# Optimization experiments

Hardware: AMD Instinct MI355X
Metric: run time of the kernel (lower is better)

Reference implementation:

```python
import jax, jax.numpy as jnp
import numpy as np

N_HEADS = 16
EPS = 1e-6  # WanSelfAttention passes eps=1e-6 to WanRMSNorm
ROPE_MAX = 1024


def _rmsnorm(v, g):
    # WanRMSNorm: normalize in fp32 over the full `dim`, then scale by weight
    v32 = v.astype(jnp.float32)
    n = v32 * jax.lax.rsqrt(jnp.mean(v32 * v32, axis=-1, keepdims=True) + EPS)
    return n * g


def _rope(x, f, h, w, fc, fs):
    # x: [b, s, n, d] with s == f*h*w. Complex rope: (a+bi) * (cos + i sin)
    b, s, n, d = x.shape
    c = d // 2
    c1 = c - 2 * (c // 3)
    c2 = c // 3

    def build(t):  # t: [ROPE_MAX, c] -> [1, s, 1, c]
        tf, th, tw = t[:, :c1], t[:, c1:c1 + c2], t[:, c1 + c2:]
        pf = jnp.broadcast_to(tf[:f, None, None, :], (f, h, w, c1))
        ph = jnp.broadcast_to(th[None, :h, None, :], (f, h, w, c2))
        pw = jnp.broadcast_to(tw[None, None, :w, :], (f, h, w, c2))
        return jnp.concatenate([pf, ph, pw], axis=-1).reshape(1, f * h * w, 1, c)

    cosv, sinv = build(fc), build(fs)
    xr = x.astype(jnp.float32).reshape(b, s, n, c, 2)
    a, bi = xr[..., 0], xr[..., 1]
    out_r = a * cosv - bi * sinv
    out_i = a * sinv + bi * cosv
    return jnp.stack([out_r, out_i], axis=-1).reshape(b, s, n, d)


def setup_inputs() -> dict:
    key = jax.random.key(0)
    ks = jax.random.split(key, 12)
    b, s, dim = 1, 2048, 2048
    n, d = N_HEADS, 2048 // N_HEADS  # d = 128, c = 64
    f, h, w = 2, 32, 32              # f*h*w == s
    c = d // 2
    c1 = c - 2 * (c // 3)
    c2 = c // 3

    # Realistic rope tables per band (cos/sin of pos * inv_freq)
    pos = np.arange(ROPE_MAX, dtype=np.float64)[:, None]
    ang = []
    for cx in (c1, c2, c2):
        inv = 1.0 / (10000.0 ** (np.arange(cx, dtype=np.float64) / cx))
        ang.append(pos * inv[None, :])
    ang = np.concatenate(ang, axis=1)
    freqs_cos = jnp.asarray(np.cos(ang), dtype=jnp.float32)
    freqs_sin = jnp.asarray(np.sin(ang), dtype=jnp.float32)

    scale = 1.0 / np.sqrt(dim)
    inp = {
        "x": jax.random.normal(ks[0], (b, s, dim), dtype=jnp.float32),
        "freqs_cos": freqs_cos,
        "freqs_sin": freqs_sin,
        "Wq": jax.random.normal(ks[1], (dim, dim), dtype=jnp.float32) * scale,
        "bq": jnp.zeros((dim,), dtype=jnp.float32),
        "Wk": jax.random.normal(ks[2], (dim, dim), dtype=jnp.float32) * scale,
        "bk": jnp.zeros((dim,), dtype=jnp.float32),
        "Wv": jax.random.normal(ks[3], (dim, dim), dtype=jnp.float32) * scale,
        "bv": jnp.zeros((dim,), dtype=jnp.float32),
        "Wo": jax.random.normal(ks[4], (dim, dim), dtype=jnp.float32) * scale,
        "bo": jnp.zeros((dim,), dtype=jnp.float32),
        "gq": jnp.ones((dim,), dtype=jnp.float32),
        "gk": jnp.ones((dim,), dtype=jnp.float32),
        "seq_lens": jnp.array([s], dtype=jnp.int32),
        "f": f,
        "h": h,
        "w": w,
    }
    return inp


def reference(x, freqs_cos, freqs_sin, Wq, bq, Wk, bk, Wv, bv, Wo, bo, gq, gk,
              seq_lens, f, h, w):
    b, s, dim = x.shape
    n = N_HEADS
    d = dim // n

    q = _rmsnorm(x @ Wq.T + bq, gq).reshape(b, s, n, d)
    k = _rmsnorm(x @ Wk.T + bk, gk).reshape(b, s, n, d)
    v = (x @ Wv.T + bv).reshape(b, s, n, d)

    q = _rope(q, f, h, w, freqs_cos, freqs_sin)
    k = _rope(k, f, h, w, freqs_cos, freqs_sin)

    scale = np.float32(1.0 / np.sqrt(d))
    scores = jnp.einsum('bqnd,bknd->bnqk', q, k) * scale  # [b,n,s,s]
    key_mask = jnp.arange(s)[None, :] < seq_lens[:, None]  # [b,s] (k_lens)
    scores = jnp.where(key_mask[:, None, None, :], scores, -jnp.inf)
    probs = jax.nn.softmax(scores, axis=-1)
    out = jnp.einsum('bnqk,bknd->bqnd', probs, v).reshape(b, s, dim)
    return out @ Wo.T + bo
```

## Files before the change

kernel.cpp:

```cpp
#include <hip/hip_runtime.h>
#include <cstdint>
#include <cmath>

typedef unsigned int uint;
typedef unsigned short ushort;
typedef __bf16 bf16_t;
typedef bf16_t bf16x8 __attribute__((ext_vector_type(8)));
typedef float f32x4 __attribute__((ext_vector_type(4)));
typedef float f32x16 __attribute__((ext_vector_type(16)));

#define LOG2E 1.44269504088896340736f

__device__ __forceinline__ ushort f2bf(float f) {
  uint x = __float_as_uint(f);
  x += 0x7fffu + ((x >> 16) & 1u);
  return (ushort)(x >> 16);
}
__device__ __forceinline__ uint pack2(float lo, float hi) {
  return (uint)f2bf(lo) | ((uint)f2bf(hi) << 16);
}
__device__ __forceinline__ uint cvt_pk_bf16(float lo, float hi) {
  uint r;
  asm("v_cvt_pk_bf16_f32 %0, %1, %2" : "=v"(r) : "v"(lo), "v"(hi));
  return r;
}

__device__ __forceinline__ void gload_lds16(const void* gsrc, void* ldsdst) {
  typedef const __attribute__((address_space(1))) unsigned int* gp_t;
  typedef __attribute__((address_space(3))) unsigned int* lp_t;
  __builtin_amdgcn_global_load_lds((gp_t)(uintptr_t)gsrc,
                                   (lp_t)(unsigned int)(uintptr_t)ldsdst,
                                   16, 0, 0);
}

__global__ __launch_bounds__(256) void cvt5(const float* __restrict__ x,
                                            const float* __restrict__ wq,
                                            const float* __restrict__ wk,
                                            const float* __restrict__ wv,
                                            const float* __restrict__ wo,
                                            ushort* __restrict__ xb,
                                            ushort* __restrict__ wqkv,
                                            ushort* __restrict__ wob,
                                            int nx8, int nw8) {
  const int y = blockIdx.y;
  const float* src;
  ushort* dst;
  int n8;
  if (y == 0)      { src = x;  dst = xb;  n8 = nx8; }
  else if (y == 4) { src = wo; dst = wob; n8 = nw8; }
  else {
    src = (y == 1) ? wq : (y == 2) ? wk : wv;
    dst = wqkv + (size_t)(y - 1) * nw8 * 8;
    n8 = nw8;
  }
  int i = blockIdx.x * blockDim.x + threadIdx.x;
  if (i >= n8) return;
  const float4* s4 = (const float4*)src;
  float4 a = s4[i * 2], b = s4[i * 2 + 1];
  uint4 o;
  o.x = pack2(a.x, a.y); o.y = pack2(a.z, a.w);
  o.z = pack2(b.x, b.y); o.w = pack2(b.z, b.w);
  ((uint4*)dst)[i] = o;
}

__global__ __launch_bounds__(512) void gemm_qkv192(const ushort* __restrict__ A,
                                                   const ushort* __restrict__ B,
                                                   const float* __restrict__ bq,
                                                   const float* __restrict__ bk,
                                                   const float* __restrict__ bv,
                                                   float* __restrict__ qpre,
                                                   float* __restrict__ kpre,
                                                   ushort* __restrict__ Vt,
                                                   int K, int S_) {
  __shared__ __align__(16) unsigned char ldsA[65536];
  __shared__ __align__(16) unsigned char ldsB[49152];
  const int t = threadIdx.x, l = t & 63;
  const int w = t >> 6;
  const int g = l >> 4, c = l & 15;
  const int wr = w >> 2, wc = w & 3;
  const int tm = blockIdx.y * 256, tn = blockIdx.x * 192;

  const int srow = t >> 3;
  const int schunk = (t & 7) ^ (srow & 7);
  const ushort* Ag = A + (size_t)(tm + srow) * K + schunk * 8;
  const ushort* Bg = B + (size_t)(tn + srow) * K + schunk * 8;
  const size_t rK64 = (size_t)64 * K;

#define STG_A(kt, u) gload_lds16(Ag + (size_t)(u) * rK64 + ((kt) << 6),   \
    ldsA + ((kt)&1) * 32768 + (u) * 8192 + t * 16)
#define STG_B(kt, u) gload_lds16(Bg + (size_t)(u) * rK64 + ((kt) << 6),   \
    ldsB + ((kt)&1) * 24576 + (u) * 8192 + t * 16)

  f32x4 acc[8][3] = {};
  bf16x8 af[2][2], bfr[3][2];
  const int cr = c * 128;
  const int sw0 = ((0 * 4 + g) ^ (c & 7)) << 4;
  const int sw1 = ((1 * 4 + g) ^ (c & 7)) << 4;

#define RDA(d, q) do {                                                               \
    _Pragma("unroll") for (int mm = 0; mm < 2; ++mm) {                               \
      const unsigned char* p_ = ldsA + (d)*32768 + (wr*128 + (q)*32 + mm*16)*128 + cr; \
      af[mm][0] = *(const bf16x8*)(p_ + sw0);                                        \
      af[mm][1] = *(const bf16x8*)(p_ + sw1); }                                      \
  } while (0)
#define RDB(d) do {                                                                 \
    _Pragma("unroll") for (int nn = 0; nn < 3; ++nn) {                              \
      const unsigned char* p_ = ldsB + (d)*24576 + (wc*48 + nn*16)*128 + cr;        \
      bfr[nn][0] = *(const bf16x8*)(p_ + sw0);                                      \
      bfr[nn][1] = *(const bf16x8*)(p_ + sw1); }                                    \
  } while (0)
#define MM(q) do {                                                                  \
    __builtin_amdgcn_s_setprio(1);                                                  \
    _Pragma("unroll") for (int mm = 0; mm < 2; ++mm)                                \
    _Pragma("unroll") for (int nn = 0; nn < 3; ++nn) {                              \
      acc[(q)*2+mm][nn] = __builtin_amdgcn_mfma_f32_16x16x32_bf16(                  \
          af[mm][0], bfr[nn][0], acc[(q)*2+mm][nn], 0, 0, 0);                       \
      acc[(q)*2+mm][nn] = __builtin_amdgcn_mfma_f32_16x16x32_bf16(                  \
          af[mm][1], bfr[nn][1], acc[(q)*2+mm][nn], 0, 0, 0); }                     \
    __builtin_amdgcn_s_setprio(0);                                                  \
  } while (0)
#define BAR() __builtin_amdgcn_s_barrier()

  STG_B(0, 0); STG_B(0, 1); STG_B(0, 2);
  STG_A(0, 0); STG_A(0, 1); STG_A(0, 2); STG_A(0, 3);
  STG_B(1, 0); STG_B(1, 1); STG_B(1, 2);
  STG_A(1, 0); STG_A(1, 1); STG_A(1, 2);
  asm volatile("s_waitcnt vmcnt(6)" ::: "memory");
  BAR();

  const int NITER = K >> 7;
  for (int i = 0; i < NITER; ++i) {
    const int k1 = 2 * i + 1, k2 = 2 * i + 2, k3 = 2 * i + 3;
    const bool st = (i + 1 < NITER);
    RDA(0, 0); RDB(0);
    STG_A(k1, 3);
    MM(0); BAR();
    RDA(0, 1);
    if (st) { STG_B(k2, 0); STG_B(k2, 1); }
    MM(1); BAR();
    RDA(0, 2);
    if (st) { STG_B(k2, 2); STG_A(k2, 0); }
    MM(2); BAR();
    RDA(0, 3);
    if (st) { STG_A(k2, 1); STG_A(k2, 2); }
    MM(3);
    if (st) asm volatile("s_waitcnt vmcnt(6)" ::: "memory");
    else    asm volatile("s_waitcnt vmcnt(0)" ::: "memory");
    BAR();
    RDA(1, 0); RDB(1);
    if (st) STG_A(k2, 3);
    MM(0); BAR();
    RDA(1, 1);
    if (st) { STG_B(k3, 0); STG_B(k3, 1); }
    MM(1); BAR();
    RDA(1, 2);
    if (st) { STG_B(k3, 2); STG_A(k3, 0); }
    MM(2); BAR();
    RDA(1, 3);
    if (st) { STG_A(k3, 1); STG_A(k3, 2); }
    MM(3);
    if (st) asm volatile("s_waitcnt vmcnt(6)" ::: "memory");
    else    asm volatile("s_waitcnt vmcnt(0)" ::: "memory");
    BAR();
  }

#undef STG_A
#undef STG_B
#undef RDA
#undef RDB
#undef MM
#undef BAR

#pragma unroll
  for (int n = 0; n < 3; ++n) {
    int col = tn + wc * 48 + n * 16 + c;
    int sel = col >> 11;
    if (sel < 2) {
      float* outp = sel ? kpre : qpre;
      const float* bias = sel ? bk : bq;
      int col2 = col & 2047;
      float bvv = bias[col2];
#pragma unroll
      for (int m = 0; m < 8; ++m) {
        int row0 = tm + wr * 128 + m * 16 + g * 4;
#pragma unroll
        for (int i = 0; i < 4; ++i)
          outp[(size_t)(row0 + i) * 2048 + col2] = acc[m][n][i] + bvv;
      }
    } else {
      int colv = col - 4096;
      float bvv = bv[colv];
#pragma unroll
      for (int m = 0; m < 8; ++m) {
        int row0 = tm + wr * 128 + m * 16 + g * 4;
        uint2 o;
        o.x = pack2(acc[m][n][0] + bvv, acc[m][n][1] + bvv);
        o.y = pack2(acc[m][n][2] + bvv, acc[m][n][3] + bvv);
        *(uint2*)(Vt + (size_t)colv * S_ + row0) = o;
      }
    }
  }
}

__global__ __launch_bounds__(512) void gemm_wo_db(const ushort* __restrict__ A,
                                                  const ushort* __restrict__ B,
                                                  float* __restrict__ pbuf, int K) {
  __shared__ __align__(16) unsigned char As[16384];
  __shared__ __align__(16) unsigned char Bs[16384];
  const int t = threadIdx.x, l = t & 63, w = t >> 6;
  const int g = l >> 4, c = l & 15;
  const int wr = w >> 1, wc = w & 1;
  const int tm = blockIdx.y * 128, tn = blockIdx.x * 128;
  const int ks = blockIdx.z;
  const int k0 = ks * (K >> 1);

  const int srow = w * 16 + (l >> 2);
  const int schunk = (l & 3) ^ (srow & 3);
  const ushort* Ag = A + (size_t)(tm + srow) * K + k0 + schunk * 8;
  const ushort* Bg = B + (size_t)(tn + srow) * K + k0 + schunk * 8;

  f32x4 acc[2][4] = {};

  const int NT = K >> 6;
  gload_lds16(Ag, As + w * 1024);
  gload_lds16(Bg, Bs + w * 1024);

  for (int j = 0; j < NT; ++j) {
    const int buf = j & 1, nb = buf ^ 1;
    if (j + 1 < NT) {
      const int kt1 = (j + 1) << 5;
      gload_lds16(Ag + kt1, As + nb * 8192 + w * 1024);
      gload_lds16(Bg + kt1, Bs + nb * 8192 + w * 1024);
      asm volatile("s_waitcnt vmcnt(2)" ::: "memory");
    } else {
      asm volatile("s_waitcnt vmcnt(0)" ::: "memory");
    }
    __builtin_amdgcn_s_barrier();

    const unsigned char* Ab = As + buf * 8192;
    const unsigned char* Bb = Bs + buf * 8192;
    bf16x8 af[2], bfr[4];
#pragma unroll
    for (int m = 0; m < 2; ++m) {
      int row = wr * 32 + m * 16 + c;
      af[m] = *(const bf16x8*)(Ab + row * 64 + ((g ^ (row & 3)) << 4));
    }
#pragma unroll
    for (int n = 0; n < 4; ++n) {
      int row = wc * 64 + n * 16 + c;
      bfr[n] = *(const bf16x8*)(Bb + row * 64 + ((g ^ (row & 3)) << 4));
    }
#pragma unroll
    for (int m = 0; m < 2; ++m)
#pragma unroll
      for (int n = 0; n < 4; ++n)
        acc[m][n] = __builtin_amdgcn_mfma_f32_16x16x32_bf16(af[m], bfr[n], acc[m][n], 0, 0, 0);

    __builtin_amdgcn_s_barrier();
  }

  float* out = pbuf + (size_t)ks * 2048 * 2048;
#pragma unroll
  for (int n = 0; n < 4; ++n) {
    int col = tn + wc * 64 + n * 16 + c;
#pragma unroll
    for (int m = 0; m < 2; ++m) {
      int row0 = tm + wr * 32 + m * 16 + g * 4;
#pragma unroll
      for (int i = 0; i < 4; ++i)
        out[(size_t)(row0 + i) * 2048 + col] = acc[m][n][i];
    }
  }
}

__global__ __launch_bounds__(256) void reduce_wo(const float* __restrict__ p,
                                                 const float* __restrict__ bo,
                                                 float* __restrict__ out, int n4) {
  int i = blockIdx.x * blockDim.x + threadIdx.x;
  if (i >= n4) return;
  float4 a = ((const float4*)p)[i];
  float4 b = ((const float4*)p)[i + n4];
  float4 bb = *(const float4*)(bo + ((i * 4) & 2047));
  float4 o;
  o.x = a.x + b.x + bb.x; o.y = a.y + b.y + bb.y;
  o.z = a.z + b.z + bb.z; o.w = a.w + b.w + bb.w;
  ((float4*)out)[i] = o;
}

__global__ __launch_bounds__(256) void fuse_rms_rope(const float* __restrict__ qpre,
                                                     const float* __restrict__ kpre,
                                                     const float* __restrict__ gq,
                                                     const float* __restrict__ gk,
                                                     const float* __restrict__ fc,
                                                     const float* __restrict__ fs,
                                                     const int* __restrict__ pH,
                                                     const int* __restrict__ pW,
                                                     ushort* __restrict__ Qb,
                                                     ushort* __restrict__ Kb,
                                                     int dim, float foldq) {
  const int which = blockIdx.y;
  const float* pre = which ? kpre : qpre;
  const float* gw = which ? gk : gq;
  ushort* outp = which ? Kb : Qb;
  const float fold = which ? 1.0f : foldq;

  const int p = blockIdx.x, t = threadIdx.x;
  const float* row = pre + (size_t)p * dim;
  float v[8];
  {
    float4 a = *(const float4*)(row + t * 8);
    float4 b = *(const float4*)(row + t * 8 + 4);
    v[0] = a.x; v[1] = a.y; v[2] = a.z; v[3] = a.w;
    v[4] = b.x; v[5] = b.y; v[6] = b.z; v[7] = b.w;
  }
  float ss = 0.f;
#pragma unroll
  for (int i = 0; i < 8; ++i) ss += v[i] * v[i];
#pragma unroll
  for (int off = 32; off; off >>= 1) ss += __shfl_xor(ss, off);
  __shared__ float wsum[4];
  if ((t & 63) == 0) wsum[t >> 6] = ss;
  __syncthreads();
  float rstd = rsqrtf((wsum[0] + wsum[1] + wsum[2] + wsum[3]) * (1.0f / dim) + 1e-6f);
  float gv[8];
  {
    float4 a = *(const float4*)(gw + t * 8);
    float4 b = *(const float4*)(gw + t * 8 + 4);
    gv[0] = a.x; gv[1] = a.y; gv[2] = a.z; gv[3] = a.w;
    gv[4] = b.x; gv[5] = b.y; gv[6] = b.z; gv[7] = b.w;
  }
#pragma unroll
  for (int i = 0; i < 8; ++i) v[i] = v[i] * rstd * gv[i];

  const int H = pH[0], W = pW[0];
  const int hw = H * W;
  const int fr = p / hw;
  const int rem = p - fr * hw;
  const int hh = rem / W;
  const int ww = rem - hh * W;
  const int hd = dim / 16;
  const int cd = hd >> 1;
  const int c2 = cd / 3, c1 = cd - 2 * c2;
  const int j0 = ((t * 8) % hd) >> 1;

  uint ob[4];
#pragma unroll
  for (int q = 0; q < 4; ++q) {
    int j = j0 + q;
    int ri = (j < c1) ? fr : ((j < c1 + c2) ? hh : ww);
    float cs = fc[ri * cd + j];
    float sn = fs[ri * cd + j];
    float a = v[2 * q], b = v[2 * q + 1];
    ob[q] = pack2((a * cs - b * sn) * fold, (a * sn + b * cs) * fold);
  }
  uint4 o4; o4.x = ob[0]; o4.y = ob[1]; o4.z = ob[2]; o4.w = ob[3];
  *(uint4*)(outp + (size_t)p * dim + t * 8) = o4;
}

__global__ __launch_bounds__(512, 2) void attn32(const ushort* __restrict__ Qb,
                                                 const ushort* __restrict__ Kb,
                                                 const ushort* __restrict__ Vt,
                                                 ushort* __restrict__ Ob,
                                                 const int* __restrict__ seq_lens,
                                                 int S_, int DIMc) {
  __shared__ __align__(16) unsigned char smem[66560];
  float* mlbuf = (float*)(smem + 65536);
  const int t = threadIdx.x, l = t & 63, w = t >> 6;
  const int qsub = w & 3, ksp = w >> 2;
  const int h = l >> 5, ql = l & 31;

  const int orig = blockIdx.y * gridDim.x + blockIdx.x;
  const int nwg = gridDim.x * gridDim.y;
  const int lin = (orig & 7) * (nwg >> 3) + (orig >> 3);
  const int q0 = (lin % gridDim.x) * 128;
  const int head = lin / gridDim.x;
  const int kvlen = seq_lens[0];

  unsigned char* sk_s = smem + ksp * 16384;
  unsigned char* sv_s = smem + 32768 + ksp * 16384;

  bf16x8 qf[8];
  {
    const ushort* qp = Qb + (size_t)(q0 + qsub * 32 + ql) * DIMc + head * 128 + h * 8;
#pragma unroll
    for (int s = 0; s < 8; ++s) qf[s] = *(const bf16x8*)(qp + s * 16);
  }

  f32x16 ofr[4] = {};
  float m_run = -1e30f, l_run = 0.f;

  const int nt = (kvlen + 63) >> 6;
  const int half = (nt + 1) >> 1;
  const int tbase = ksp ? half : 0;
  const int mycnt = ksp ? (nt - half) : half;

  for (int tt = 0; tt < half; ++tt) {
    __syncthreads();
    if (tt < mycnt) {
      const int kv0 = (tbase + tt) * 64;
#pragma unroll
      for (int it = 0; it < 4; ++it) {
        int kr = qsub * 16 + it * 4 + (l >> 4);
        int kc = (l & 15) ^ (kr & 15);
        gload_lds16(Kb + (size_t)(kv0 + kr) * DIMc + head * 128 + kc * 8,
                    sk_s + qsub * 4096 + it * 1024);
        int vr = qsub * 32 + it * 8 + (l >> 3);
        int vc = (l & 7) ^ (vr & 7);
        gload_lds16(Vt + (size_t)(head * 128 + vr) * S_ + kv0 + vc * 8,
                    sv_s + qsub * 4096 + it * 1024);
      }
    }
    __syncthreads();
    if (tt >= mycnt) continue;
    const int kv0 = (tbase + tt) * 64;

    f32x16 sfr[2] = {};
    __builtin_amdgcn_s_setprio(1);
#pragma unroll
    for (int kb = 0; kb < 2; ++kb) {
      const unsigned char* kbp = sk_s + (kb * 32 + ql) * 256;
      const int rx = (kb * 32 + ql) & 15;
#pragma unroll
      for (int s = 0; s < 8; ++s) {
        bf16x8 kf = *(const bf16x8*)(kbp + (((s * 2 + h) ^ rx) << 4));
        sfr[kb] = __builtin_amdgcn_mfma_f32_32x32x16_bf16(kf, qf[s], sfr[kb], 0, 0, 0);
      }
    }
    __builtin_amdgcn_s_setprio(0);

    if (kv0 + 64 > kvlen) {
#pragma unroll
      for (int kb = 0; kb < 2; ++kb)
#pragma unroll
        for (int r = 0; r < 16; ++r) {
          int key = kv0 + kb * 32 + (r & 3) + 8 * (r >> 2) + 4 * h;
          if (key >= kvlen) sfr[kb][r] = -1e30f;
        }
    }

    float mt = -1e30f;
#pragma unroll
    for (int kb = 0; kb < 2; ++kb)
#pragma unroll
      for (int r = 0; r < 16; ++r) mt = fmaxf(mt, sfr[kb][r]);
    mt = fmaxf(mt, __shfl_xor(mt, 32));

    if (!__all(mt <= m_run + 8.0f)) {
      float m_new = fmaxf(m_run, mt);
      float fac = __builtin_amdgcn_exp2f(m_run - m_new);
      l_run *= fac;
#pragma unroll
      for (int df = 0; df < 4; ++df) ofr[df] *= fac;
      m_run = m_new;
    }

    float ls = 0.f;
    uint u[2][4][2];
#pragma unroll
    for (int kb = 0; kb < 2; ++kb)
#pragma unroll
      for (int G = 0; G < 4; ++G) {
        float p0 = __builtin_amdgcn_exp2f(sfr[kb][G * 4 + 0] - m_run);
        float p1 = __builtin_amdgcn_exp2f(sfr[kb][G * 4 + 1] - m_run);
        float p2 = __builtin_amdgcn_exp2f(sfr[kb][G * 4 + 2] - m_run);
        float p3 = __builtin_amdgcn_exp2f(sfr[kb][G * 4 + 3] - m_run);
        ls += (p0 + p1) + (p2 + p3);
        u[kb][G][0] = cvt_pk_bf16(p0, p1);
        u[kb][G][1] = cvt_pk_bf16(p2, p3);
      }
    ls += __shfl_xor(ls, 32);
    l_run += ls;

#pragma unroll
    for (int ks = 0; ks < 4; ++ks) {
      const int kb = ks >> 1, G0 = (ks & 1) * 2;
      uint own0 = h ? u[kb][G0 + 1][0] : u[kb][G0][0];
      uint own1 = h ? u[kb][G0 + 1][1] : u[kb][G0][1];
      uint snd0 = h ? u[kb][G0][0] : u[kb][G0 + 1][0];
      uint snd1 = h ? u[kb][G0][1] : u[kb][G0 + 1][1];
      uint rcv0 = __shfl_xor(snd0, 32);
      uint rcv1 = __shfl_xor(snd1, 32);
      union { uint4 q; bf16x8 b; } uu;
      uu.q.x = h ? rcv0 : own0;
      uu.q.y = h ? rcv1 : own1;
      uu.q.z = h ? own0 : rcv0;
      uu.q.w = h ? own1 : rcv1;
      __builtin_amdgcn_s_setprio(1);
#pragma unroll
      for (int df = 0; df < 4; ++df) {
        const int row = df * 32 + ql;
        bf16x8 vf = *(const bf16x8*)(sv_s + row * 128 + (((ks * 2 + h) ^ (row & 7)) << 4));
        ofr[df] = __builtin_amdgcn_mfma_f32_32x32x16_bf16(vf, uu.b, ofr[df], 0, 0, 0);
      }
      __builtin_amdgcn_s_setprio(0);
    }
  }

  __syncthreads();
  if (ksp == 1) {
    if (h == 0) { mlbuf[qsub * 64 + ql] = m_run; mlbuf[qsub * 64 + 32 + ql] = l_run; }
    float* ob = (float*)(smem + qsub * 16384);
#pragma unroll
    for (int df = 0; df < 4; ++df)
#pragma unroll
      for (int r = 0; r < 16; ++r) {
        int d = df * 32 + (r & 3) + 8 * (r >> 2) + 4 * h;
        ob[d * 32 + ql] = ofr[df][r];
      }
  }
  __syncthreads();
  if (ksp == 0) {
    float m2 = mlbuf[qsub * 64 + ql], l2 = mlbuf[qsub * 64 + 32 + ql];
    float mstar = fmaxf(m_run, m2);
    float f1 = __builtin_amdgcn_exp2f(m_run - mstar);
    float f2 = (l2 > 0.f) ? __builtin_amdgcn_exp2f(m2 - mstar) : 0.f;
    float lstar = l_run * f1 + l2 * f2;
    float inv = 1.0f / lstar;
    float a1 = f1 * inv, a2 = f2 * inv;
    const float* ob = (const float*)(smem + qsub * 16384);
    ushort* orow = Ob + (size_t)(q0 + qsub * 32 + ql) * DIMc + head * 128;
#pragma unroll
    for (int df = 0; df < 4; ++df)
#pragma unroll
      for (int G = 0; G < 4; ++G) {
        int d0 = df * 32 + 8 * G + 4 * h;
        float v0 = ofr[df][G * 4 + 0] * a1 + ob[(d0 + 0) * 32 + ql] * a2;
        float v1 = ofr[df][G * 4 + 1] * a1 + ob[(d0 + 1) * 32 + ql] * a2;
        float v2 = ofr[df][G * 4 + 2] * a1 + ob[(d0 + 2) * 32 + ql] * a2;
        float v3 = ofr[df][G * 4 + 3] * a1 + ob[(d0 + 3) * 32 + ql] * a2;
        uint2 o; o.x = pack2(v0, v1); o.y = pack2(v2, v3);
        *(uint2*)(orow + d0) = o;
      }
  }
}

extern "C" void kernel_launch(void* const* d_in, const int* in_sizes, int n_in,
                              void* d_out, int out_size, void* d_ws, size_t ws_size,
                              hipStream_t stream) {
  const float* x  = (const float*)d_in[0];
  const float* fc = (const float*)d_in[1];
  const float* fs = (const float*)d_in[2];
  const float* Wq = (const float*)d_in[3];
  const float* bq = (const float*)d_in[4];
  const float* Wk = (const float*)d_in[5];
  const float* bk = (const float*)d_in[6];
  const float* Wv = (const float*)d_in[7];
  const float* bv = (const float*)d_in[8];
  const float* Wo = (const float*)d_in[9];
  const float* bo = (const float*)d_in[10];
  const float* gq = (const float*)d_in[11];
  const float* gk = (const float*)d_in[12];
  const int* seq  = (const int*)d_in[13];
  const int* pH   = (const int*)d_in[15];
  const int* pW   = (const int*)d_in[16];

  const int DIMc = in_sizes[4];
  const int S_   = in_sizes[0] / DIMc;

  char* ws = (char*)d_ws;
  const size_t MB = 1024ull * 1024ull;
  ushort* xb    = (ushort*)(ws + 0 * MB);
  ushort* Wqkvb = (ushort*)(ws + 8 * MB);
  ushort* Wob   = (ushort*)(ws + 32 * MB);
  float*  qpre  = (float*)(ws + 40 * MB);
  float*  kpre  = (float*)(ws + 56 * MB);
  ushort* Qb    = (ushort*)(ws + 72 * MB);
  ushort* Kb    = (ushort*)(ws + 80 * MB);
  ushort* Vt    = (ushort*)(ws + 88 * MB);
  ushort* Ob    = (ushort*)(ws + 40 * MB);
  float*  pbuf  = (float*)(ws + 56 * MB);

  const int nx8 = (S_ * DIMc) / 8;
  const int nw8 = (DIMc * DIMc) / 8;
  const int nmax = (nx8 > nw8 ? nx8 : nw8);
  cvt5<<<dim3((nmax + 255) / 256, 5), 256, 0, stream>>>(x, Wq, Wk, Wv, Wo,
                                                        xb, Wqkvb, Wob, nx8, nw8);

  gemm_qkv192<<<dim3(3 * DIMc / 192, S_ / 256), 512, 0, stream>>>(
      xb, Wqkvb, bq, bk, bv, qpre, kpre, Vt, DIMc, S_);

  const float foldq = LOG2E / sqrtf((float)(DIMc / 16));
  fuse_rms_rope<<<dim3(S_, 2), 256, 0, stream>>>(qpre, kpre, gq, gk, fc, fs, pH, pW,
                                                 Qb, Kb, DIMc, foldq);

  attn32<<<dim3(S_ / 128, 16), 512, 0, stream>>>(Qb, Kb, Vt, Ob, seq, S_, DIMc);

  gemm_wo_db<<<dim3(16, 16, 2), 512, 0, stream>>>(Ob, Wob, pbuf, DIMc);
  reduce_wo<<<(S_ * DIMc / 4 + 255) / 256, 256, 0, stream>>>(pbuf, bo, (float*)d_out,
                                                             S_ * DIMc / 4);
}
```

Before: 172.2 us.

## Prefetch next K/V tile into registers while computing current tile

Replaces direct global-to-LDS loads in the attention loop with register staging. The next tile's K and V are loaded into registers while the current tile is computed, then written to LDS at the top of the next iteration. Address computation is hoisted out of the loop and the barriers become raw s_barrier calls with an explicit lgkmcnt wait. The aim is to hide global memory latency behind the MFMA work. The cost is extra VGPRs, which may lower occupancy, and reliance on hand-placed waits for correctness.

```diff
diff --git a/kernel.cpp b/kernel.cpp
--- a/kernel.cpp
+++ b/kernel.cpp
@@ -394,23 +394,49 @@
   const int tbase = ksp ? half : 0;
   const int mycnt = ksp ? (nt - half) : half;
 
+  const ushort* kbase[4];
+  const ushort* vbase[4];
+  uint4* kdst[4];
+  uint4* vdst[4];
+#pragma unroll
+  for (int it = 0; it < 4; ++it) {
+    int kr = qsub * 16 + it * 4 + (l >> 4);
+    int kc = (l & 15) ^ (kr & 15);
+    kbase[it] = Kb + (size_t)kr * DIMc + head * 128 + kc * 8;
+    kdst[it] = (uint4*)(sk_s + qsub * 4096 + it * 1024 + l * 16);
+    int vr = qsub * 32 + it * 8 + (l >> 3);
+    int vc = (l & 7) ^ (vr & 7);
+    vbase[it] = Vt + (size_t)(head * 128 + vr) * S_ + vc * 8;
+    vdst[it] = (uint4*)(sv_s + qsub * 4096 + it * 1024 + l * 16);
+  }
+
+  uint4 kreg[4], vreg[4];
+  if (mycnt > 0) {
+    const int kv0 = tbase * 64;
+#pragma unroll
+    for (int it = 0; it < 4; ++it) {
+      kreg[it] = *(const uint4*)(kbase[it] + (size_t)kv0 * DIMc);
+      vreg[it] = *(const uint4*)(vbase[it] + kv0);
+    }
+  }
+
   for (int tt = 0; tt < half; ++tt) {
-    __syncthreads();
+    __builtin_amdgcn_s_barrier();
     if (tt < mycnt) {
-      const int kv0 = (tbase + tt) * 64;
-#pragma unroll
-      for (int it = 0; it < 4; ++it) {
-        int kr = qsub * 16 + it * 4 + (l >> 4);
-        int kc = (l & 15) ^ (kr & 15);
-        gload_lds16(Kb + (size_t)(kv0 + kr) * DIMc + head * 128 + kc * 8,
-                    sk_s + qsub * 4096 + it * 1024);
-        int vr = qsub * 32 + it * 8 + (l >> 3);
-        int vc = (l & 7) ^ (vr & 7);
-        gload_lds16(Vt + (size_t)(head * 128 + vr) * S_ + kv0 + vc * 8,
-                    sv_s + qsub * 4096 + it * 1024);
-      }
-    }
-    __syncthreads();
+#pragma unroll
+      for (int it = 0; it < 4; ++it) { *kdst[it] = kreg[it]; *vdst[it] = vreg[it]; }
+      if (tt + 1 < mycnt) {
+        const int kv0n = (tbase + tt + 1) * 64;
+#pragma unroll
+        for (int it = 0; it < 4; ++it) {
+          kreg[it] = *(const uint4*)(kbase[it] + (size_t)kv0n * DIMc);
+          vreg[it] = *(const uint4*)(vbase[it] + kv0n);
+        }
+      }
+    }
+    asm volatile("s_waitcnt lgkmcnt(0)" ::: "memory");
+    __builtin_amdgcn_s_barrier();
+    __builtin_amdgcn_sched_barrier(0);
     if (tt >= mycnt) continue;
     const int kv0 = (tbase + tt) * 64;
 
```

Result: slower. 228.1 us (+32.5%).

## Prefetch next K/V tile into registers to overlap global loads with compute

Applied to the files above, without the earlier changes.

Replaces the direct global-to-LDS loads of K and V tiles in the attention loop with register prefetching. The next tile is loaded into registers while the current tile is processed, then written to LDS at the top of the next iteration. Address offsets are precomputed outside the loop. This hides global memory latency behind the MFMA work, at the cost of extra VGPRs and an explicit LDS store step, which may reduce occupancy.

```diff
diff --git a/kernel.cpp b/kernel.cpp
--- a/kernel.cpp
+++ b/kernel.cpp
@@ -394,23 +394,56 @@
   const int tbase = ksp ? half : 0;
   const int mycnt = ksp ? (nt - half) : half;
 
+#define MKK(IT, KO, KD) size_t KO; uint KD;                                     \
+  { int kr_ = qsub * 16 + (IT) * 4 + (l >> 4); int kc_ = (l & 15) ^ (kr_ & 15); \
+    KO = (size_t)kr_ * DIMc + head * 128 + kc_ * 8;                             \
+    KD = (uint)(ksp * 16384 + qsub * 4096 + (IT) * 1024 + l * 16); }
+#define MKV(IT, VO, VD) size_t VO; uint VD;                                     \
+  { int vr_ = qsub * 32 + (IT) * 8 + (l >> 3); int vc_ = (l & 7) ^ (vr_ & 7);   \
+    VO = (size_t)(head * 128 + vr_) * S_ + vc_ * 8;                             \
+    VD = (uint)(32768 + ksp * 16384 + qsub * 4096 + (IT) * 1024 + l * 16); }
+  MKK(0, kO0, kD0) MKK(1, kO1, kD1) MKK(2, kO2, kD2) MKK(3, kO3, kD3)
+  MKV(0, vO0, vD0) MKV(1, vO1, vD1) MKV(2, vO2, vD2) MKV(3, vO3, vD3)
+#undef MKK
+#undef MKV
+
+  uint4 rk0, rk1, rk2, rk3, rv0, rv1, rv2, rv3;
+  if (mycnt > 0) {
+    const size_t kbq = (size_t)(tbase * 64) * DIMc;
+    const int vq = tbase * 64;
+    rk0 = *(const uint4*)(Kb + kO0 + kbq);
+    rk1 = *(const uint4*)(Kb + kO1 + kbq);
+    rk2 = *(const uint4*)(Kb + kO2 + kbq);
+    rk3 = *(const uint4*)(Kb + kO3 + kbq);
+    rv0 = *(const uint4*)(Vt + vO0 + vq);
+    rv1 = *(const uint4*)(Vt + vO1 + vq);
+    rv2 = *(const uint4*)(Vt + vO2 + vq);
+    rv3 = *(const uint4*)(Vt + vO3 + vq);
+  }
+
   for (int tt = 0; tt < half; ++tt) {
-    __syncthreads();
+    __builtin_amdgcn_s_barrier();
     if (tt < mycnt) {
-      const int kv0 = (tbase + tt) * 64;
-#pragma unroll
-      for (int it = 0; it < 4; ++it) {
-        int kr = qsub * 16 + it * 4 + (l >> 4);
-        int kc = (l & 15) ^ (kr & 15);
-        gload_lds16(Kb + (size_t)(kv0 + kr) * DIMc + head * 128 + kc * 8,
-                    sk_s + qsub * 4096 + it * 1024);
-        int vr = qsub * 32 + it * 8 + (l >> 3);
-        int vc = (l & 7) ^ (vr & 7);
-        gload_lds16(Vt + (size_t)(head * 128 + vr) * S_ + kv0 + vc * 8,
-                    sv_s + qsub * 4096 + it * 1024);
-      }
-    }
-    __syncthreads();
+      *(uint4*)(smem + kD0) = rk0; *(uint4*)(smem + kD1) = rk1;
+      *(uint4*)(smem + kD2) = rk2; *(uint4*)(smem + kD3) = rk3;
+      *(uint4*)(smem + vD0) = rv0; *(uint4*)(smem + vD1) = rv1;
+      *(uint4*)(smem + vD2) = rv2; *(uint4*)(smem + vD3) = rv3;
+      if (tt + 1 < mycnt) {
+        const size_t kbq = (size_t)((tbase + tt + 1) * 64) * DIMc;
+        const int vq = (tbase + tt + 1) * 64;
+        rk0 = *(const uint4*)(Kb + kO0 + kbq);
+        rk1 = *(const uint4*)(Kb + kO1 + kbq);
+        rk2 = *(const uint4*)(Kb + kO2 + kbq);
+        rk3 = *(const uint4*)(Kb + kO3 + kbq);
+        rv0 = *(const uint4*)(Vt + vO0 + vq);
+        rv1 = *(const uint4*)(Vt + vO1 + vq);
+        rv2 = *(const uint4*)(Vt + vO2 + vq);
+        rv3 = *(const uint4*)(Vt + vO3 + vq);
+      }
+    }
+    asm volatile("s_waitcnt lgkmcnt(0)" ::: "memory");
+    __builtin_amdgcn_s_barrier();
+    __builtin_amdgcn_sched_barrier(0);
     if (tt >= mycnt) continue;
     const int kv0 = (tbase + tt) * 64;
 
```

Result: faster. 167.3 us (-2.9%).
